# Performance work log

Measured on AMD Instinct MI355X. Metric: run time of the kernel, lower is better.

The kernel has to match this reference:

```python
import jax, jax.numpy as jnp
import numpy as np

N_IMG = 256; N_PAD = 512; N_DELAYS = 32; N_GRID = 512
PIX = 4e-5; L_IMG = N_IMG * PIX
R_BODY = 0.008; V0 = 1500.0; GRID_HALF = 0.02
N_TH = 240; N_INT = 250; W0 = 30.0
LAM_TV = 1e-3; LAM_L1 = 1e-3

def _fourier_coord(n, l):
    f = np.fft.fftshift(np.fft.fftfreq(n, d=l / n))
    kx, ky = np.meshgrid(f, f, indexing='ij')
    k = 2.0 * np.pi * np.sqrt(kx ** 2 + ky ** 2)
    theta = np.mod(np.arctan2(ky, kx), 2.0 * np.pi)
    return k.astype(np.float32), theta.astype(np.float32)

_K2D, _TH2D = _fourier_coord(N_PAD, 2.0 * L_IMG)
K2D = jnp.asarray(_K2D)[None, None]            # [1,1,P,P]
TH2D = jnp.asarray(_TH2D)                      # [P,P]
MASK0 = jnp.asarray(((_TH2D >= 0.0) & (_TH2D <= 2 * np.pi)).astype(np.float32))
_THPI = np.mod(_TH2D + np.pi, 2 * np.pi)
MASK1 = jnp.asarray(((_THPI >= 0.0) & (_THPI <= 2 * np.pi)).astype(np.float32))
K_LOSS = jnp.asarray(np.fft.ifftshift(_K2D))[None, None]
_SIG = 0.0015 / PIX / np.sqrt(2.0 * np.log(2.0))   # gaussian window sigma (pixels)
_AX = np.arange(N_IMG) - (N_IMG - 1) / 2.0
_G = np.exp(-_AX ** 2 / (2.0 * _SIG ** 2))
GWIN = jnp.asarray(np.outer(_G, _G).astype(np.float32))[None]   # [1,N,N]
THETAS_WF = jnp.linspace(0.0, 2.0 * np.pi, N_TH, dtype=jnp.float32)   # [T]
STEPS = jnp.linspace(0.0, 1.0, N_INT, dtype=jnp.float32)[None]        # [1,S]


def _interp1d(xg, yg, xn):
    # linear interp on uniform grid xg (1D) of values yg; xn arbitrary shape
    dxg = xg[1] - xg[0]
    t = (xn - xg[0]) / dxg
    f = jnp.clip(jnp.floor(t).astype(jnp.int32), 0, xg.shape[0] - 1)
    c = jnp.clip(jnp.ceil(t).astype(jnp.int32), 0, xg.shape[0] - 1)
    yf, yc = yg[f], yg[c]
    denom = jnp.where(c == f, 1.0, xg[c] - xg[f])
    lin = yf + (yc - yf) * (xn - xg[f]) / denom
    return jnp.where(c == f, yc, lin)


def _wavefront(xq, yq, SoS, x_vec, y_vec):
    # time-of-flight wavefront: trapezoid quadrature of (1 - v0/SoS) along rays
    r = jnp.sqrt(xq ** 2 + yq ** 2)
    phi = jnp.arctan2(xq, yq)
    th = THETAS_WF[:, None]                      # [T,1]
    s = jnp.sin(th - phi)
    cd = jnp.cos(th - phi)                       # cos(phi - th) == cos(th - phi)
    disc = jnp.maximum(R_BODY ** 2 - (r * s) ** 2, 0.0)
    l_in = jnp.sqrt(disc) + r * cd
    l_out = 2.0 * jnp.sqrt(disc) * (cd >= 0.0).astype(jnp.float32)
    l = jnp.where(r < R_BODY, l_in, l_out)       # [T,1]
    dx = x_vec[1] - x_vec[0]
    dy = y_vec[1] - y_vec[0]
    xi = jnp.round((xq - l * STEPS * jnp.sin(th) - x_vec[0]) / dx).astype(jnp.int32)
    yi = jnp.round((yq - l * STEPS * jnp.cos(th) - y_vec[0]) / dy).astype(jnp.int32)
    fint = 1.0 - V0 / SoS[(-yi) % N_GRID, xi % N_GRID]   # [T,S] gather
    xs = l * STEPS                               # [T,S]
    wf = jnp.sum(0.5 * (fint[:, 1:] + fint[:, :-1]) * (xs[:, 1:] - xs[:, :-1]), axis=1)
    return THETAS_WF, wf


def _tf_pact(delays, thetas, wfs):
    w = _interp1d(thetas, wfs, TH2D)
    w_pi = _interp1d(thetas, wfs, jnp.mod(TH2D + jnp.pi, 2.0 * jnp.pi))
    d = delays.reshape(1, -1, 1, 1)
    tf = (jnp.exp(-1j * K2D * (d - w)) * MASK0 + jnp.exp(1j * K2D * (d - w_pi)) * MASK1) * 0.5
    return jnp.fft.ifftshift(tf, axes=(-2, -1))  # [1,D,P,P] complex


def _siren(x, W1, b1, W2, b2, W3, b3, W4, b4):
    h = jnp.sin(W0 * (x @ W1 + b1))
    h = jnp.sin(W0 * (h @ W2 + b2))
    h = jnp.sin(W0 * (h @ W3 + b3))
    return h @ W4 + b4


def _forward(W1, b1, W2, b2, W3, b3, W4, b4, y_img, delays, xq, yq,
             mgrid_masked, mask, mask_idx, x_vec, y_vec):
    out = _siren(mgrid_masked, W1, b1, W2, b2, W3, b3, W4, b4)[:, 0]
    SoS = jnp.full((N_GRID * N_GRID,), 1499.363, jnp.float32)
    SoS = SoS.at[mask_idx].set(out * 170.0 + 1550.0).reshape(N_GRID, N_GRID)
    thetas, wfs = _wavefront(xq[0], yq[0], SoS, x_vec, y_vec)
    H = _tf_pact(delays, thetas, wfs)
    yw = y_img * GWIN                                  # [1,D,N,N]
    pad = N_IMG // 2
    yp = jnp.pad(yw, ((0, 0), (0, 0), (pad, pad), (pad, pad)))
    Y = jnp.fft.fft2(jnp.fft.ifftshift(yp, axes=(-2, -1)))
    Ht = jnp.conj(H)
    HtH = jnp.abs(H) ** 2
    rhs = jnp.sum(Y * Ht, axis=-3, keepdims=True)
    lhs = jnp.sum(HtH, axis=-3, keepdims=True)
    X = rhs / lhs
    x_rec = jnp.fft.fftshift(jnp.fft.ifft2(X), axes=(-2, -1)).real
    data = jnp.mean((jnp.abs(Y) * K_LOSS - jnp.abs(H * X) * K_LOSS) ** 2, axis=(-3, -2, -1))
    tv = LAM_TV * (jnp.sum(jnp.abs((SoS[1:, :] - SoS[:-1, :]) * mask[1:, :]))
                   + jnp.sum(jnp.abs((SoS[:, 1:] - SoS[:, :-1]) * mask[:, 1:])))
    l1 = LAM_L1 * jnp.mean(jnp.abs(SoS - 1550.0) * mask)
    loss = data + tv + l1
    return x_rec, SoS, loss


def setup_inputs() -> dict:
    key = jax.random.key(0)
    ks = jax.random.split(key, 12)
    xg = np.linspace(-GRID_HALF, GRID_HALF, N_GRID).astype(np.float32)
    XX, YY = np.meshgrid(xg, xg, indexing='ij')
    mask_np = (XX ** 2 + YY ** 2 <= R_BODY ** 2).astype(np.float32)
    mask_idx = np.nonzero(mask_np.reshape(-1))[0].astype(np.int32)
    lin = np.linspace(-1.0, 1.0, N_GRID).astype(np.float32)
    GX, GY = np.meshgrid(lin, lin, indexing='ij')
    mgrid = np.stack([GX, GY], axis=-1).reshape(-1, 2)
    H = 128
    c = np.sqrt(6.0 / H) / W0
    def u(k, shape, b):
        return jax.random.uniform(k, shape, jnp.float32, -b, b)
    return {
        'W1': u(ks[0], (2, H), 0.5), 'b1': u(ks[1], (H,), 0.5),
        'W2': u(ks[2], (H, H), c), 'b2': u(ks[3], (H,), c),
        'W3': u(ks[4], (H, H), c), 'b3': u(ks[5], (H,), c),
        'W4': u(ks[6], (H, 1), c), 'b4': u(ks[7], (1,), c),
        'y_img': jax.random.normal(ks[8], (1, N_DELAYS, N_IMG, N_IMG), jnp.float32),
        'delays': jax.random.normal(ks[9], (N_DELAYS,), jnp.float32) * 5e-4,
        'xq': jnp.array([0.002], jnp.float32),
        'yq': jnp.array([0.001], jnp.float32),
        'mgrid_masked': jnp.asarray(mgrid[mask_idx]),
        'mask': jnp.asarray(mask_np),
        'mask_idx': jnp.asarray(mask_idx),
        'x_vec': jnp.asarray(xg),
        'y_vec': jnp.asarray(xg),
    }


def reference(W1, b1, W2, b2, W3, b3, W4, b4, y_img, delays, xq, yq,
              mgrid_masked, mask, mask_idx, x_vec, y_vec):
    return _forward(W1, b1, W2, b2, W3, b3, W4, b4, y_img, delays, xq, yq,
                    mgrid_masked, mask, mask_idx, x_vec, y_vec)
```

## Files before the change

kernel.cpp:

```cpp
#include <hip/hip_runtime.h>
#include <hip/hip_bf16.h>
#include <math.h>

#define NP 512
#define NIMG 256
#define NDEL 32
#define NTH 240
#define NINT 250
#define SOS_ELEMS (512*512)
#define MLP_P 32
#define PHY(i) ((i) + ((i) >> 3))
#define RSW 576
#define PI_F 3.14159265358979323846f

__device__ __forceinline__ int brev9(int i) { return (int)(__brev((unsigned)i) >> 23); }

__device__ __forceinline__ float block_reduce_any(float v) {
  #pragma unroll
  for (int o = 32; o > 0; o >>= 1) v += __shfl_down(v, o, 64);
  __shared__ float red[8];
  int lane = threadIdx.x & 63, wid = threadIdx.x >> 6;
  __syncthreads();
  if (lane == 0) red[wid] = v;
  __syncthreads();
  float r = 0.f;
  if (threadIdx.x == 0) {
    int nw = blockDim.x >> 6;
    for (int i = 0; i < nw; ++i) r += red[i];
  }
  return r;
}

__device__ __forceinline__ void r4_bfly(float2& x0, float2& x1, float2& x2, float2& x3,
                                        float c1, float s1n, float c2, float s2n, float sign) {
  float t1x = x1.x * c1 - x1.y * s1n, t1y = x1.x * s1n + x1.y * c1;
  float y0x = x0.x + t1x, y0y = x0.y + t1y;
  float y1x = x0.x - t1x, y1y = x0.y - t1y;
  float t3x = x3.x * c1 - x3.y * s1n, t3y = x3.x * s1n + x3.y * c1;
  float y2x = x2.x + t3x, y2y = x2.y + t3y;
  float y3x = x2.x - t3x, y3y = x2.y - t3y;
  float t2x = y2x * c2 - y2y * s2n, t2y = y2x * s2n + y2y * c2;
  float ux = y3x * c2 - y3y * s2n, uy = y3x * s2n + y3y * c2;
  float t4x = -sign * uy, t4y = sign * ux;
  x0 = make_float2(y0x + t2x, y0y + t2y);
  x2 = make_float2(y0x - t2x, y0y - t2y);
  x1 = make_float2(y1x + t4x, y1y + t4y);
  x3 = make_float2(y1x - t4x, y1y - t4y);
}

__device__ __forceinline__ void fft512_r4_fwd_rows(float2 (*s)[RSW], int tid) {
  #pragma unroll
  for (int pass = 0; pass < 4; ++pass) {
    const int sh = 2 * pass;
    const int h = 1 << sh;
    int p = tid & 127;
    int rbase = (tid >> 7) << 2;
    int j = p & (h - 1);
    int g = p >> sh;
    int base = (g << (sh + 2)) + j;
    int i0 = PHY(base), i1 = PHY(base + h), i2 = PHY(base + 2 * h), i3 = PHY(base + 3 * h);
    float ang1 = -PI_F * (float)j / (float)h;
    float s1n, c1; __sincosf(ang1, &s1n, &c1);
    float s2n, c2; __sincosf(0.5f * ang1, &s2n, &c2);
    #pragma unroll
    for (int rr = 0; rr < 4; ++rr) {
      int r = rbase + rr;
      float2 x0 = s[r][i0], x1 = s[r][i1], x2 = s[r][i2], x3 = s[r][i3];
      r4_bfly(x0, x1, x2, x3, c1, s1n, c2, s2n, -1.f);
      s[r][i0] = x0; s[r][i1] = x1; s[r][i2] = x2; s[r][i3] = x3;
    }
    __syncthreads();
  }
  {
    int p = tid;
    int i1 = PHY(p), i2 = PHY(p + 256);
    float ang = -PI_F * (float)p * (1.f / 256.f);
    float sn, cs; __sincosf(ang, &sn, &cs);
    #pragma unroll
    for (int r = 0; r < 8; ++r) {
      float2 a = s[r][i1], b = s[r][i2];
      float tr = b.x * cs - b.y * sn;
      float ti = b.x * sn + b.y * cs;
      s[r][i1] = make_float2(a.x + tr, a.y + ti);
      s[r][i2] = make_float2(a.x - tr, a.y - ti);
    }
    __syncthreads();
  }
}

__device__ __forceinline__ void fft512_r4_fwd_rows4(float2 (*s)[RSW], int tid) {
  #pragma unroll
  for (int pass = 0; pass < 4; ++pass) {
    const int sh = 2 * pass;
    const int h = 1 << sh;
    int p = tid & 127;
    int rbase = (tid >> 7) << 1;
    int j = p & (h - 1);
    int g = p >> sh;
    int base = (g << (sh + 2)) + j;
    int i0 = PHY(base), i1 = PHY(base + h), i2 = PHY(base + 2 * h), i3 = PHY(base + 3 * h);
    float ang1 = -PI_F * (float)j / (float)h;
    float s1n, c1; __sincosf(ang1, &s1n, &c1);
    float s2n, c2; __sincosf(0.5f * ang1, &s2n, &c2);
    #pragma unroll
    for (int rr = 0; rr < 2; ++rr) {
      int r = rbase + rr;
      float2 x0 = s[r][i0], x1 = s[r][i1], x2 = s[r][i2], x3 = s[r][i3];
      r4_bfly(x0, x1, x2, x3, c1, s1n, c2, s2n, -1.f);
      s[r][i0] = x0; s[r][i1] = x1; s[r][i2] = x2; s[r][i3] = x3;
    }
    __syncthreads();
  }
  {
    int p = tid;
    int i1 = PHY(p), i2 = PHY(p + 256);
    float ang = -PI_F * (float)p * (1.f / 256.f);
    float sn, cs; __sincosf(ang, &sn, &cs);
    #pragma unroll
    for (int r = 0; r < 4; ++r) {
      float2 a = s[r][i1], b = s[r][i2];
      float tr = b.x * cs - b.y * sn;
      float ti = b.x * sn + b.y * cs;
      s[r][i1] = make_float2(a.x + tr, a.y + ti);
      s[r][i2] = make_float2(a.x - tr, a.y - ti);
    }
    __syncthreads();
  }
}

__device__ __forceinline__ void fft512_r4_row(float2* s, int tid, float sign) {
  #pragma unroll
  for (int pass = 0; pass < 4; ++pass) {
    const int sh = 2 * pass;
    const int h = 1 << sh;
    if (tid < 128) {
      int j = tid & (h - 1);
      int g = tid >> sh;
      int base = (g << (sh + 2)) + j;
      int i0 = PHY(base), i1 = PHY(base + h), i2 = PHY(base + 2 * h), i3 = PHY(base + 3 * h);
      float ang1 = sign * PI_F * (float)j / (float)h;
      float s1n, c1; __sincosf(ang1, &s1n, &c1);
      float s2n, c2; __sincosf(0.5f * ang1, &s2n, &c2);
      float2 x0 = s[i0], x1 = s[i1], x2 = s[i2], x3 = s[i3];
      r4_bfly(x0, x1, x2, x3, c1, s1n, c2, s2n, sign);
      s[i0] = x0; s[i1] = x1; s[i2] = x2; s[i3] = x3;
    }
    __syncthreads();
  }
  {
    int i1 = PHY(tid), i2 = PHY(tid + 256);
    float ang = sign * PI_F * (float)tid * (1.f / 256.f);
    float sn, cs; __sincosf(ang, &sn, &cs);
    float2 a = s[i1], b = s[i2];
    float tr = b.x * cs - b.y * sn;
    float ti = b.x * sn + b.y * cs;
    s[i1] = make_float2(a.x + tr, a.y + ti);
    s[i2] = make_float2(a.x - tr, a.y - ti);
    __syncthreads();
  }
}

__global__ __launch_bounds__(128) void k_mlp(
    const float* __restrict__ W1, const float* __restrict__ b1,
    const float* __restrict__ W2, const float* __restrict__ b2,
    const float* __restrict__ W3, const float* __restrict__ b3,
    const float* __restrict__ W4v, const float* __restrict__ b4,
    const float* __restrict__ mgrid, const int* __restrict__ mask_idx,
    const float* __restrict__ mask, int M,
    float* __restrict__ sos, float* __restrict__ acc) {
  __shared__ float hbuf[MLP_P][132];
  __shared__ float wbuf[2][8][132];
  __shared__ float xy2[MLP_P][2];
  int tid = threadIdx.x;
  int base = blockIdx.x * MLP_P;
  if (tid < MLP_P * 2) {
    int p = tid >> 1, c = tid & 1;
    float v = 0.f;
    if (base + p < M) v = mgrid[(base + p) * 2 + c];
    xy2[p][c] = v;
  }
  if (blockIdx.x == 0 && tid < 4) acc[tid] = 0.f;
  for (int slab = blockIdx.x; slab < 1024; slab += gridDim.x) {
    #pragma unroll
    for (int e = 0; e < 2; ++e) {
      int t = slab * 256 + tid + e * 128;
      if (mask[t] == 0.f) sos[t] = 1499.363f;
    }
  }
  __syncthreads();
  for (int e = tid; e < MLP_P * 128; e += 128) {
    int p = e >> 7, j = e & 127;
    hbuf[p][j] = __sinf(30.f * (xy2[p][0] * W1[j] + xy2[p][1] * W1[128 + j] + b1[j]));
  }
  __syncthreads();

  int jg = tid & 15, pg = tid >> 4;
  int jA = jg * 4, jB = 64 + jg * 4;
  int p0 = pg * 4;
  int wr = tid >> 4, wc = (tid & 15) << 3;
  #pragma unroll
  for (int layer = 0; layer < 2; ++layer) {
    const float* Wg = layer ? W3 : W2;
    const float* bb = layer ? b3 : b2;
    float acr[4][8];
    #pragma unroll
    for (int i = 0; i < 4; ++i)
      #pragma unroll
      for (int j = 0; j < 8; ++j) acr[i][j] = 0.f;

    float4 pre1 = *(const float4*)&Wg[wr * 128 + wc];
    float4 pre2 = *(const float4*)&Wg[wr * 128 + wc + 4];
    for (int c = 0; c < 16; ++c) {
      *(float4*)&wbuf[c & 1][wr][wc] = pre1;
      *(float4*)&wbuf[c & 1][wr][wc + 4] = pre2;
      __syncthreads();
      if (c < 15) {
        pre1 = *(const float4*)&Wg[((c + 1) * 8 + wr) * 128 + wc];
        pre2 = *(const float4*)&Wg[((c + 1) * 8 + wr) * 128 + wc + 4];
      }
      int k0 = c * 8;
      float hreg[4][8];
      #pragma unroll
      for (int i = 0; i < 4; ++i) {
        float4 ha = *(const float4*)&hbuf[p0 + i][k0];
        float4 hb = *(const float4*)&hbuf[p0 + i][k0 + 4];
        hreg[i][0] = ha.x; hreg[i][1] = ha.y; hreg[i][2] = ha.z; hreg[i][3] = ha.w;
        hreg[i][4] = hb.x; hreg[i][5] = hb.y; hreg[i][6] = hb.z; hreg[i][7] = hb.w;
      }
      #pragma unroll
      for (int kk = 0; kk < 8; ++kk) {
        float4 wa = *(const float4*)&wbuf[c & 1][kk][jA];
        float4 wb = *(const float4*)&wbuf[c & 1][kk][jB];
        float w8[8] = {wa.x, wa.y, wa.z, wa.w, wb.x, wb.y, wb.z, wb.w};
        #pragma unroll
        for (int i = 0; i < 4; ++i) {
          float hv = hreg[i][kk];
          #pragma unroll
          for (int j = 0; j < 8; ++j) acr[i][j] += hv * w8[j];
        }
      }
    }
    float breg[8];
    #pragma unroll
    for (int j = 0; j < 4; ++j) { breg[j] = bb[jA + j]; breg[4 + j] = bb[jB + j]; }
    __syncthreads();
    #pragma unroll
    for (int i = 0; i < 4; ++i) {
      float o[8];
      #pragma unroll
      for (int j = 0; j < 8; ++j) o[j] = __sinf(30.f * (acr[i][j] + breg[j]));
      *(float4*)&hbuf[p0 + i][jA] = make_float4(o[0], o[1], o[2], o[3]);
      *(float4*)&hbuf[p0 + i][jB] = make_float4(o[4], o[5], o[6], o[7]);
    }
    __syncthreads();
  }
  {
    int p = tid >> 2, q = tid & 3;
    float s = 0.f;
    #pragma unroll
    for (int k = 0; k < 32; k += 4) {
      float4 h4 = *(const float4*)&hbuf[p][q * 32 + k];
      float4 w4 = *(const float4*)&W4v[q * 32 + k];
      s += h4.x * w4.x + h4.y * w4.y + h4.z * w4.z + h4.w * w4.w;
    }
    s += __shfl_down(s, 1, 64);
    s += __shfl_down(s, 2, 64);
    if (q == 0 && base + p < M)
      sos[mask_idx[base + p]] = (s + b4[0]) * 170.f + 1550.f;
  }
}

__global__ __launch_bounds__(256) void k_mid(
    const float* __restrict__ y_img, float2* __restrict__ bufA,
    const float* __restrict__ sos, const float* __restrict__ xq_p,
    const float* __restrict__ yq_p, const float* __restrict__ x_vec,
    const float* __restrict__ y_vec, float* __restrict__ wfs,
    const float* __restrict__ mask, float* __restrict__ acc) {
  __shared__ float2 s[4][RSW];
  int bid = blockIdx.x;
  int tid = threadIdx.x;
  if (bid < 1024) {
    int rt = bid & 31;
    int d = bid >> 5;
    const float INV2S2 = (float)(0.6931471805599453 / 1406.25);
    for (int e = tid; e < 2048; e += 256) {
      int i = e >> 8, c = e & 255;
      int r = rt * 8 + i;
      float axr = (float)r - 127.5f;
      float axc = (float)c - 127.5f;
      float g = __expf(-(axr * axr + axc * axc) * INV2S2);
      float val = y_img[((size_t)d << 16) + (r << 8) + c] * g;
      int p = i >> 1, comp = i & 1;
      ((float*)&s[p][PHY(brev9((c + 384) & 511))])[comp] = val;
      ((float*)&s[p][PHY(brev9(c + 128))])[comp] = 0.f;
    }
    __syncthreads();
    fft512_r4_fwd_rows4(s, tid);
    float2* outp = bufA + ((size_t)d << 17) + rt * 8;
    for (int e = tid; e < 2056; e += 256) {
      int i = e & 7, v = e >> 3;
      int p = i >> 1, comp = i & 1;
      float2 Zv = s[p][PHY(v)];
      float2 Zm = s[p][PHY((512 - v) & 511)];
      float2 Yv;
      if (comp == 0) Yv = make_float2(0.5f * (Zv.x + Zm.x), 0.5f * (Zv.y - Zm.y));
      else           Yv = make_float2(0.5f * (Zv.y + Zm.y), 0.5f * (Zm.x - Zv.x));
      outp[(size_t)v * 256 + i] = Yv;
    }
  } else if (bid < 1024 + NTH) {
    int i = bid - 1024;
    int j = tid;
    float xq = xq_p[0], yq = yq_p[0];
    float r = sqrtf(xq * xq + yq * yq);
    float phi = atan2f(xq, yq);
    float th = (float)((double)i * (2.0 * M_PI / 239.0));
    float sn = sinf(th - phi), cd = cosf(th - phi);
    const float R2 = 0.008f * 0.008f;
    float disc = fmaxf(R2 - (r * sn) * (r * sn), 0.f);
    float sq = sqrtf(disc);
    float l_in = sq + r * cd;
    float l_out = 2.f * sq * (cd >= 0.f ? 1.f : 0.f);
    float l = (r < 0.008f) ? l_in : l_out;
    float x0 = x_vec[0], dx = x_vec[1] - x_vec[0];
    float y0 = y_vec[0], dy = y_vec[1] - y_vec[0];
    float sinth = sinf(th), costh = cosf(th);
    float contrib = 0.f;
    if (j < NINT) {
      float sj = (float)j * (1.f / 249.f);
      int xi = (int)rintf((xq - l * sj * sinth - x0) / dx);
      int yi = (int)rintf((yq - l * sj * costh - y0) / dy);
      float sv = sos[(((-yi) & 511) << 9) + (xi & 511)];
      float f = 1.f - 1500.f / sv;
      float wgt = (j == 0 || j == NINT - 1) ? 0.5f : 1.f;
      contrib = wgt * f;
    }
    float tot = block_reduce_any(contrib);
    if (tid == 0) wfs[i] = tot * l * (1.f / 249.f);
  } else {
    int t = (bid - 1024 - NTH) * 256 + tid;
    float sv = sos[t];
    float m = mask[t];
    int i = t >> 9, j = t & 511;
    float tv = 0.f;
    if (i > 0) tv += fabsf((sv - sos[t - 512]) * m);
    if (j > 0) tv += fabsf((sv - sos[t - 1]) * m);
    float l1 = fabsf(sv - 1550.f) * m;
    float tvb = block_reduce_any(tv);
    float l1b = block_reduce_any(l1);
    if (tid == 0) {
      atomicAdd(&acc[1], tvb);
      atomicAdd(&acc[2], l1b);
    }
  }
}

__device__ __forceinline__ float interp_wf(const float* wfs, float xn) {
  const float dxg = (float)(2.0 * M_PI / 239.0);
  float t = xn / dxg;
  int f = (int)floorf(t); f = min(max(f, 0), 239);
  int c = (int)ceilf(t);  c = min(max(c, 0), 239);
  float yf = wfs[f], yc = wfs[c];
  if (c == f) return yc;
  float xgf = (float)f * dxg;
  return yf + (yc - yf) * (xn - xgf) / ((float)(c - f) * dxg);
}

__global__ __launch_bounds__(256) void k_colfft_deconv(
    const float2* __restrict__ bufA, const float* __restrict__ delays,
    const float* __restrict__ wfs_g, float2* __restrict__ Xo,
    float* __restrict__ acc) {
  __shared__ float2 s[8][RSW];
  __shared__ float wfs[NTH];
  __shared__ float dly[NDEL];
  int v = blockIdx.x;
  int tid = threadIdx.x;
  if (tid < NTH) wfs[tid] = wfs_g[tid];
  if (tid < NDEL) dly[tid] = delays[tid];
  __syncthreads();

  const float inv_nd = 1.f / 0.02048f;
  const float TWO_PI = 6.28318530717958647692f;
  float fy = (float)(v < 256 ? v : v - 512) * inv_nd;
  float kkA[2];
  float2 zw[2], zwpi[2];
  int up[2];
  #pragma unroll
  for (int uu = 0; uu < 2; ++uu) {
    int u = tid + 256 * uu;
    up[uu] = PHY(u);
    float fx = (float)(u < 256 ? u : u - 512) * inv_nd;
    float kk = TWO_PI * sqrtf(fx * fx + fy * fy);
    kkA[uu] = kk;
    float th = atan2f(fy, fx);
    if (th < 0.f) th += TWO_PI;
    float w = interp_wf(wfs, th);
    float thpi = th + PI_F;
    if (thpi >= TWO_PI) thpi -= TWO_PI;
    float wpi = interp_wf(wfs, thpi);
    float snw, csw; __sincosf(kk * w, &snw, &csw);
    zw[uu] = make_float2(csw, snw);
    float snp, csp; __sincosf(kk * wpi, &snp, &csp);
    zwpi[uu] = make_float2(csp, snp);
  }

  float rhsr[2] = {0.f, 0.f}, rhsi[2] = {0.f, 0.f}, lhs[2] = {0.f, 0.f};
  float sY2[2] = {0.f, 0.f}, sYH[2] = {0.f, 0.f};

  for (int c4 = 0; c4 < 4; ++c4) {
    __syncthreads();
    for (int e = tid; e < 2048; e += 256) {
      int ch = e >> 8, c = e & 255;
      float2 val = bufA[((size_t)(c4 * 8 + ch) << 17) + (size_t)v * 256 + c];
      s[ch][PHY(brev9((c + 384) & 511))] = val;
      s[ch][PHY(brev9(c + 128))] = make_float2(0.f, 0.f);
    }
    __syncthreads();
    fft512_r4_fwd_rows(s, tid);
    #pragma unroll
    for (int uu = 0; uu < 2; ++uu) {
      float kk = kkA[uu];
      float2 w0 = zw[uu], w1 = zwpi[uu];
      #pragma unroll
      for (int ch = 0; ch < 8; ++ch) {
        float dl = dly[c4 * 8 + ch];
        float sd, cd2;
        __sincosf(kk * dl, &sd, &cd2);
        float t0r = cd2 * w0.x + sd * w0.y;
        float t0i = cd2 * w0.y - sd * w0.x;
        float t1r = cd2 * w1.x + sd * w1.y;
        float t1i = sd * w1.x - cd2 * w1.y;
        float Hr = 0.5f * (t0r + t1r);
        float Hi = 0.5f * (t0i + t1i);
        float2 Yv = s[ch][up[uu]];
        rhsr[uu] += Yv.x * Hr + Yv.y * Hi;
        rhsi[uu] += Yv.y * Hr - Yv.x * Hi;
        float h2 = Hr * Hr + Hi * Hi;
        float y2 = Yv.x * Yv.x + Yv.y * Yv.y;
        lhs[uu] += h2;
        sY2[uu] += y2;
        sYH[uu] += sqrtf(y2 * h2);
      }
    }
  }
  float lw = (v == 0 || v == 256) ? 1.f : 2.f;
  float2 Xv[2];
  float lsum = 0.f;
  #pragma unroll
  for (int uu = 0; uu < 2; ++uu) {
    float Xr = rhsr[uu] / lhs[uu], Xi = rhsi[uu] / lhs[uu];
    Xv[uu] = make_float2(Xr, Xi);
    float aX = sqrtf(Xr * Xr + Xi * Xi);
    float kk2 = kkA[uu] * kkA[uu];
    lsum += kk2 * (sY2[uu] - 2.f * aX * sYH[uu] + aX * aX * lhs[uu]);
  }
  float bs = block_reduce_any(lsum * lw);
  if (threadIdx.x == 0) atomicAdd(&acc[0], bs);
  __syncthreads();
  float2* s0 = &s[0][0];
  s0[PHY(brev9(tid))] = Xv[0];
  s0[PHY(brev9(tid + 256))] = Xv[1];
  __syncthreads();
  fft512_r4_row(s0, tid, +1.f);
  const float sc = 1.f / 512.f;
  float2 o0 = s0[PHY(tid)], o1 = s0[PHY(tid + 256)];
  o0.x *= sc; o0.y *= sc; o1.x *= sc; o1.y *= sc;
  Xo[((size_t)tid << 9) + v] = o0;
  Xo[((size_t)(tid + 256) << 9) + v] = o1;
  if (v != 0 && v != 256) {
    int vm = 512 - v;
    Xo[((size_t)tid << 9) + vm] = make_float2(o0.x, -o0.y);
    Xo[((size_t)(tid + 256) << 9) + vm] = make_float2(o1.x, -o1.y);
  }
}

__global__ __launch_bounds__(256) void k_final_rows(const float2* __restrict__ buf,
                                                    float* __restrict__ xrec,
                                                    const float* __restrict__ acc,
                                                    float* __restrict__ lossout) {
  __shared__ float2 s[RSW];
  int arow = blockIdx.x;
  const float2* p = buf + ((size_t)arow << 9);
  int tid = threadIdx.x;
  if (arow == 0 && tid == 0)
    lossout[0] = acc[0] * (1.f / 8388608.f) + 1e-3f * acc[1] + 1e-3f * (acc[2] * (1.f / 262144.f));
  s[PHY(brev9(tid))] = p[tid];
  s[PHY(brev9(tid + 256))] = p[tid + 256];
  __syncthreads();
  fft512_r4_row(s, tid, +1.f);
  int orow = (arow + 256) & 511;
  const float sc = 1.f / 512.f;
  xrec[(orow << 9) + ((tid + 256) & 511)] = s[PHY(tid)].x * sc;
  xrec[(orow << 9) + (tid & 511)] = s[PHY(tid + 256)].x * sc;
}

extern "C" void kernel_launch(void* const* d_in, const int* in_sizes, int n_in,
                              void* d_out, int out_size, void* d_ws, size_t ws_size,
                              hipStream_t stream) {
  const float* W1 = (const float*)d_in[0];
  const float* b1 = (const float*)d_in[1];
  const float* W2 = (const float*)d_in[2];
  const float* b2 = (const float*)d_in[3];
  const float* W3 = (const float*)d_in[4];
  const float* b3 = (const float*)d_in[5];
  const float* W4 = (const float*)d_in[6];
  const float* b4 = (const float*)d_in[7];
  const float* y_img = (const float*)d_in[8];
  const float* delays = (const float*)d_in[9];
  const float* xq = (const float*)d_in[10];
  const float* yq = (const float*)d_in[11];
  const float* mgrid = (const float*)d_in[12];
  const float* mask = (const float*)d_in[13];
  const int* mask_idx = (const int*)d_in[14];
  const float* x_vec = (const float*)d_in[15];
  const float* y_vec = (const float*)d_in[16];
  const int M = in_sizes[14];
  const int nMlp = (M + MLP_P - 1) / MLP_P;

  float* out = (float*)d_out;
  float* xrec = out;
  float* sos = out + SOS_ELEMS;
  float* loss = out + 2 * SOS_ELEMS;

  char* wsb = (char*)d_ws;
  float* acc = (float*)wsb;
  float* wfs = (float*)(wsb + 1024);
  float2* bufA = (float2*)(wsb + 4096);
  float2* bufX = (float2*)(wsb + 4096 + (size_t)NDEL * 512 * 256 * sizeof(float2));

  k_mlp<<<nMlp, 128, 0, stream>>>(W1, b1, W2, b2, W3, b3, W4, b4,
                                  mgrid, mask_idx, mask, M, sos, acc);
  k_mid<<<1024 + NTH + 1024, 256, 0, stream>>>(y_img, bufA, sos, xq, yq,
                                               x_vec, y_vec, wfs, mask, acc);
  k_colfft_deconv<<<257, 256, 0, stream>>>(bufA, delays, wfs, bufX, acc);
  k_final_rows<<<512, 256, 0, stream>>>(bufX, xrec, acc, loss);
}
```

Before: 205.5 us.

## Process four delay groups concurrently per block in column FFT deconvolution

The column-FFT deconvolution kernel now launches 1024 threads per block, so four thread groups each load and FFT one group of 8 delay channels in parallel. Previously one 256-thread block looped over the four groups in sequence. The per-group partial sums go through shared memory and are combined, and the inverse FFT is done on a single row by the first 256 threads. The aim is more parallelism and better latency hiding for the 257-block grid, which underfills the GPU. The cost is 4x shared memory (about 147KB) per block, which may exceed the LDS limit or allow only one block per CU, plus idle threads during the reduction and inverse FFT.

```diff
diff --git a/kernel.cpp b/kernel.cpp
--- a/kernel.cpp
+++ b/kernel.cpp
@@ -18,7 +18,7 @@
 __device__ __forceinline__ float block_reduce_any(float v) {
   #pragma unroll
   for (int o = 32; o > 0; o >>= 1) v += __shfl_down(v, o, 64);
-  __shared__ float red[8];
+  __shared__ float red[16];
   int lane = threadIdx.x & 63, wid = threadIdx.x >> 6;
   __syncthreads();
   if (lane == 0) red[wid] = v;
@@ -48,13 +48,13 @@
   x3 = make_float2(y1x - t4x, y1y - t4y);
 }
 
-__device__ __forceinline__ void fft512_r4_fwd_rows(float2 (*s)[RSW], int tid) {
+__device__ __forceinline__ void fft512_r4_fwd_rows(float2 (*s)[RSW], int lt) {
   #pragma unroll
   for (int pass = 0; pass < 4; ++pass) {
     const int sh = 2 * pass;
     const int h = 1 << sh;
-    int p = tid & 127;
-    int rbase = (tid >> 7) << 2;
+    int p = lt & 127;
+    int rbase = (lt >> 7) << 2;
     int j = p & (h - 1);
     int g = p >> sh;
     int base = (g << (sh + 2)) + j;
@@ -72,7 +72,7 @@
     __syncthreads();
   }
   {
-    int p = tid;
+    int p = lt;
     int i1 = PHY(p), i2 = PHY(p + 256);
     float ang = -PI_F * (float)p * (1.f / 256.f);
     float sn, cs; __sincosf(ang, &sn, &cs);
@@ -365,17 +365,19 @@
   return yf + (yc - yf) * (xn - xgf) / ((float)(c - f) * dxg);
 }
 
-__global__ __launch_bounds__(256) void k_colfft_deconv(
+__global__ __launch_bounds__(1024) void k_colfft_deconv(
     const float2* __restrict__ bufA, const float* __restrict__ delays,
     const float* __restrict__ wfs_g, float2* __restrict__ Xo,
     float* __restrict__ acc) {
-  __shared__ float2 s[8][RSW];
+  __shared__ float2 s[4][8][RSW];
   __shared__ float wfs[NTH];
   __shared__ float dly[NDEL];
   int v = blockIdx.x;
   int tid = threadIdx.x;
+  int grp = tid >> 8;
+  int lt = tid & 255;
   if (tid < NTH) wfs[tid] = wfs_g[tid];
-  if (tid < NDEL) dly[tid] = delays[tid];
+  if (tid >= 512 && tid < 512 + NDEL) dly[tid - 512] = delays[tid - 512];
   __syncthreads();
 
   const float inv_nd = 1.f / 0.02048f;
@@ -386,7 +388,7 @@
   int up[2];
   #pragma unroll
   for (int uu = 0; uu < 2; ++uu) {
-    int u = tid + 256 * uu;
+    int u = lt + 256 * uu;
     up[uu] = PHY(u);
     float fx = (float)(u < 256 ? u : u - 512) * inv_nd;
     float kk = TWO_PI * sqrtf(fx * fx + fy * fy);
@@ -403,73 +405,124 @@
     zwpi[uu] = make_float2(csp, snp);
   }
 
+  const int c4 = grp;
+  for (int e = lt; e < 2048; e += 256) {
+    int ch = e >> 8, c = e & 255;
+    float2 val = bufA[((size_t)(c4 * 8 + ch) << 17) + (size_t)v * 256 + c];
+    s[grp][ch][PHY(brev9((c + 384) & 511))] = val;
+    s[grp][ch][PHY(brev9(c + 128))] = make_float2(0.f, 0.f);
+  }
+  __syncthreads();
+  fft512_r4_fwd_rows(s[grp], lt);
+
   float rhsr[2] = {0.f, 0.f}, rhsi[2] = {0.f, 0.f}, lhs[2] = {0.f, 0.f};
   float sY2[2] = {0.f, 0.f}, sYH[2] = {0.f, 0.f};
-
-  for (int c4 = 0; c4 < 4; ++c4) {
-    __syncthreads();
-    for (int e = tid; e < 2048; e += 256) {
-      int ch = e >> 8, c = e & 255;
-      float2 val = bufA[((size_t)(c4 * 8 + ch) << 17) + (size_t)v * 256 + c];
-      s[ch][PHY(brev9((c + 384) & 511))] = val;
-      s[ch][PHY(brev9(c + 128))] = make_float2(0.f, 0.f);
-    }
-    __syncthreads();
-    fft512_r4_fwd_rows(s, tid);
+  #pragma unroll
+  for (int uu = 0; uu < 2; ++uu) {
+    float kk = kkA[uu];
+    float2 w0 = zw[uu], w1 = zwpi[uu];
+    #pragma unroll
+    for (int ch = 0; ch < 8; ++ch) {
+      float dl = dly[c4 * 8 + ch];
+      float sd, cd2;
+      __sincosf(kk * dl, &sd, &cd2);
+      float t0r = cd2 * w0.x + sd * w0.y;
+      float t0i = cd2 * w0.y - sd * w0.x;
+      float t1r = cd2 * w1.x + sd * w1.y;
+      float t1i = sd * w1.x - cd2 * w1.y;
+      float Hr = 0.5f * (t0r + t1r);
+      float Hi = 0.5f * (t0i + t1i);
+      float2 Yv = s[grp][ch][up[uu]];
+      rhsr[uu] += Yv.x * Hr + Yv.y * Hi;
+      rhsi[uu] += Yv.y * Hr - Yv.x * Hi;
+      float h2 = Hr * Hr + Hi * Hi;
+      float y2 = Yv.x * Yv.x + Yv.y * Yv.y;
+      lhs[uu] += h2;
+      sY2[uu] += y2;
+      sYH[uu] += sqrtf(y2 * h2);
+    }
+  }
+  __syncthreads();
+
+  float* rb = (float*)&s[0][0][0];
+  #pragma unroll
+  for (int uu = 0; uu < 2; ++uu) {
+    int u = lt + 256 * uu;
+    rb[(grp * 5 + 0) * 512 + u] = rhsr[uu];
+    rb[(grp * 5 + 1) * 512 + u] = rhsi[uu];
+    rb[(grp * 5 + 2) * 512 + u] = lhs[uu];
+    rb[(grp * 5 + 3) * 512 + u] = sY2[uu];
+    rb[(grp * 5 + 4) * 512 + u] = sYH[uu];
+  }
+  __syncthreads();
+
+  float lw = (v == 0 || v == 256) ? 1.f : 2.f;
+  float lsum = 0.f;
+  float2 Xv[2];
+  if (tid < 256) {
     #pragma unroll
     for (int uu = 0; uu < 2; ++uu) {
-      float kk = kkA[uu];
-      float2 w0 = zw[uu], w1 = zwpi[uu];
+      int u = lt + 256 * uu;
+      float R = 0.f, I = 0.f, L = 0.f, Y2 = 0.f, YH = 0.f;
       #pragma unroll
-      for (int ch = 0; ch < 8; ++ch) {
-        float dl = dly[c4 * 8 + ch];
-        float sd, cd2;
-        __sincosf(kk * dl, &sd, &cd2);
-        float t0r = cd2 * w0.x + sd * w0.y;
-        float t0i = cd2 * w0.y - sd * w0.x;
-        float t1r = cd2 * w1.x + sd * w1.y;
-        float t1i = sd * w1.x - cd2 * w1.y;
-        float Hr = 0.5f * (t0r + t1r);
-        float Hi = 0.5f * (t0i + t1i);
-        float2 Yv = s[ch][up[uu]];
-        rhsr[uu] += Yv.x * Hr + Yv.y * Hi;
-        rhsi[uu] += Yv.y * Hr - Yv.x * Hi;
-        float h2 = Hr * Hr + Hi * Hi;
-        float y2 = Yv.x * Yv.x + Yv.y * Yv.y;
-        lhs[uu] += h2;
-        sY2[uu] += y2;
-        sYH[uu] += sqrtf(y2 * h2);
+      for (int g = 0; g < 4; ++g) {
+        R  += rb[(g * 5 + 0) * 512 + u];
+        I  += rb[(g * 5 + 1) * 512 + u];
+        L  += rb[(g * 5 + 2) * 512 + u];
+        Y2 += rb[(g * 5 + 3) * 512 + u];
+        YH += rb[(g * 5 + 4) * 512 + u];
       }
-    }
-  }
-  float lw = (v == 0 || v == 256) ? 1.f : 2.f;
-  float2 Xv[2];
-  float lsum = 0.f;
-  #pragma unroll
-  for (int uu = 0; uu < 2; ++uu) {
-    float Xr = rhsr[uu] / lhs[uu], Xi = rhsi[uu] / lhs[uu];
-    Xv[uu] = make_float2(Xr, Xi);
-    float aX = sqrtf(Xr * Xr + Xi * Xi);
-    float kk2 = kkA[uu] * kkA[uu];
-    lsum += kk2 * (sY2[uu] - 2.f * aX * sYH[uu] + aX * aX * lhs[uu]);
+      float Xr = R / L, Xi = I / L;
+      Xv[uu] = make_float2(Xr, Xi);
+      float aX = sqrtf(Xr * Xr + Xi * Xi);
+      float kk2 = kkA[uu] * kkA[uu];
+      lsum += kk2 * (Y2 - 2.f * aX * YH + aX * aX * L);
+    }
   }
   float bs = block_reduce_any(lsum * lw);
-  if (threadIdx.x == 0) atomicAdd(&acc[0], bs);
-  __syncthreads();
-  float2* s0 = &s[0][0];
-  s0[PHY(brev9(tid))] = Xv[0];
-  s0[PHY(brev9(tid + 256))] = Xv[1];
-  __syncthreads();
-  fft512_r4_row(s0, tid, +1.f);
-  const float sc = 1.f / 512.f;
-  float2 o0 = s0[PHY(tid)], o1 = s0[PHY(tid + 256)];
-  o0.x *= sc; o0.y *= sc; o1.x *= sc; o1.y *= sc;
-  Xo[((size_t)tid << 9) + v] = o0;
-  Xo[((size_t)(tid + 256) << 9) + v] = o1;
-  if (v != 0 && v != 256) {
-    int vm = 512 - v;
-    Xo[((size_t)tid << 9) + vm] = make_float2(o0.x, -o0.y);
-    Xo[((size_t)(tid + 256) << 9) + vm] = make_float2(o1.x, -o1.y);
+  if (tid == 0) atomicAdd(&acc[0], bs);
+
+  float2* s3 = &s[3][0][0];
+  if (tid < 256) {
+    s3[PHY(brev9(lt))] = Xv[0];
+    s3[PHY(brev9(lt + 256))] = Xv[1];
+  }
+  __syncthreads();
+  #pragma unroll
+  for (int pass = 0; pass < 4; ++pass) {
+    const int sh = 2 * pass;
+    const int h = 1 << sh;
+    if (tid < 128) {
+      int j = tid & (h - 1);
+      int g = tid >> sh;
+      int base = (g << (sh + 2)) + j;
+      int i0 = PHY(base), i1 = PHY(base + h), i2 = PHY(base + 2 * h), i3 = PHY(base + 3 * h);
+      float ang1 = PI_F * (float)j / (float)h;
+      float s1n, c1; __sincosf(ang1, &s1n, &c1);
+      float s2n, c2; __sincosf(0.5f * ang1, &s2n, &c2);
+      float2 x0 = s3[i0], x1 = s3[i1], x2 = s3[i2], x3 = s3[i3];
+      r4_bfly(x0, x1, x2, x3, c1, s1n, c2, s2n, +1.f);
+      s3[i0] = x0; s3[i1] = x1; s3[i2] = x2; s3[i3] = x3;
+    }
+    __syncthreads();
+  }
+  if (tid < 256) {
+    int i1 = PHY(lt), i2 = PHY(lt + 256);
+    float ang = PI_F * (float)lt * (1.f / 256.f);
+    float sn, cs; __sincosf(ang, &sn, &cs);
+    float2 a = s3[i1], b = s3[i2];
+    float tr = b.x * cs - b.y * sn;
+    float ti = b.x * sn + b.y * cs;
+    const float sc = 1.f / 512.f;
+    float2 o0 = make_float2((a.x + tr) * sc, (a.y + ti) * sc);
+    float2 o1 = make_float2((a.x - tr) * sc, (a.y - ti) * sc);
+    Xo[((size_t)lt << 9) + v] = o0;
+    Xo[((size_t)(lt + 256) << 9) + v] = o1;
+    if (v != 0 && v != 256) {
+      int vm = 512 - v;
+      Xo[((size_t)lt << 9) + vm] = make_float2(o0.x, -o0.y);
+      Xo[((size_t)(lt + 256) << 9) + vm] = make_float2(o1.x, -o1.y);
+    }
   }
 }
 
@@ -531,6 +584,6 @@
                                   mgrid, mask_idx, mask, M, sos, acc);
   k_mid<<<1024 + NTH + 1024, 256, 0, stream>>>(y_img, bufA, sos, xq, yq,
                                                x_vec, y_vec, wfs, mask, acc);
-  k_colfft_deconv<<<257, 256, 0, stream>>>(bufA, delays, wfs, bufX, acc);
+  k_colfft_deconv<<<257, 1024, 0, stream>>>(bufA, delays, wfs, bufX, acc);
   k_final_rows<<<512, 256, 0, stream>>>(bufX, xrec, acc, loss);
 }
```

New measurement: 206.2 us. No clear change (+0.3%).

## Split column-FFT deconvolution across delay groups with a separate finalize kernel

Applied to the files above, without the earlier changes.

The single column-FFT deconvolution kernel is split in two. The first kernel launches one block per (column, group of 8 delays), 1028 blocks instead of 257, and writes its partial sums in place into the input buffer: rhs real and imaginary parts, lhs, and the YH term. A second kernel adds the four partial sums, solves for X, finishes the loss term and runs the inverse column FFT. The aim is to replace the serial four-iteration channel loop in each block with more blocks, filling the GPU better. The cost is an extra launch and several MB of extra global traffic for the partial buffers.

```diff
diff --git a/kernel.cpp b/kernel.cpp
--- a/kernel.cpp
+++ b/kernel.cpp
@@ -18,7 +18,7 @@
 __device__ __forceinline__ float block_reduce_any(float v) {
   #pragma unroll
   for (int o = 32; o > 0; o >>= 1) v += __shfl_down(v, o, 64);
-  __shared__ float red[8];
+  __shared__ float red[16];
   int lane = threadIdx.x & 63, wid = threadIdx.x >> 6;
   __syncthreads();
   if (lane == 0) red[wid] = v;
@@ -48,13 +48,13 @@
   x3 = make_float2(y1x - t4x, y1y - t4y);
 }
 
-__device__ __forceinline__ void fft512_r4_fwd_rows(float2 (*s)[RSW], int tid) {
+__device__ __forceinline__ void fft512_r4_fwd_rows(float2 (*s)[RSW], int lt) {
   #pragma unroll
   for (int pass = 0; pass < 4; ++pass) {
     const int sh = 2 * pass;
     const int h = 1 << sh;
-    int p = tid & 127;
-    int rbase = (tid >> 7) << 2;
+    int p = lt & 127;
+    int rbase = (lt >> 7) << 2;
     int j = p & (h - 1);
     int g = p >> sh;
     int base = (g << (sh + 2)) + j;
@@ -72,7 +72,7 @@
     __syncthreads();
   }
   {
-    int p = tid;
+    int p = lt;
     int i1 = PHY(p), i2 = PHY(p + 256);
     float ang = -PI_F * (float)p * (1.f / 256.f);
     float sn, cs; __sincosf(ang, &sn, &cs);
@@ -365,17 +365,19 @@
   return yf + (yc - yf) * (xn - xgf) / ((float)(c - f) * dxg);
 }
 
-__global__ __launch_bounds__(256) void k_colfft_deconv(
-    const float2* __restrict__ bufA, const float* __restrict__ delays,
-    const float* __restrict__ wfs_g, float2* __restrict__ Xo,
+__global__ __launch_bounds__(256) void k_colfft_part(
+    float2* bufA,
+    const float* __restrict__ delays, const float* __restrict__ wfs_g,
     float* __restrict__ acc) {
   __shared__ float2 s[8][RSW];
   __shared__ float wfs[NTH];
-  __shared__ float dly[NDEL];
-  int v = blockIdx.x;
+  __shared__ float dly[8];
+  int b = blockIdx.x;
+  int v = b >> 2;
+  int h = b & 3;
   int tid = threadIdx.x;
   if (tid < NTH) wfs[tid] = wfs_g[tid];
-  if (tid < NDEL) dly[tid] = delays[tid];
+  if (tid < 8) dly[tid] = delays[h * 8 + tid];
   __syncthreads();
 
   const float inv_nd = 1.f / 0.02048f;
@@ -403,66 +405,100 @@
     zwpi[uu] = make_float2(csp, snp);
   }
 
+  for (int e = tid; e < 2048; e += 256) {
+    int ch = e >> 8, c = e & 255;
+    float2 val = bufA[((size_t)(h * 8 + ch) << 17) + (size_t)v * 256 + c];
+    s[ch][PHY(brev9((c + 384) & 511))] = val;
+    s[ch][PHY(brev9(c + 128))] = make_float2(0.f, 0.f);
+  }
+  __syncthreads();
+  fft512_r4_fwd_rows(s, tid);
+
   float rhsr[2] = {0.f, 0.f}, rhsi[2] = {0.f, 0.f}, lhs[2] = {0.f, 0.f};
   float sY2[2] = {0.f, 0.f}, sYH[2] = {0.f, 0.f};
-
-  for (int c4 = 0; c4 < 4; ++c4) {
-    __syncthreads();
-    for (int e = tid; e < 2048; e += 256) {
-      int ch = e >> 8, c = e & 255;
-      float2 val = bufA[((size_t)(c4 * 8 + ch) << 17) + (size_t)v * 256 + c];
-      s[ch][PHY(brev9((c + 384) & 511))] = val;
-      s[ch][PHY(brev9(c + 128))] = make_float2(0.f, 0.f);
-    }
-    __syncthreads();
-    fft512_r4_fwd_rows(s, tid);
-    #pragma unroll
-    for (int uu = 0; uu < 2; ++uu) {
-      float kk = kkA[uu];
-      float2 w0 = zw[uu], w1 = zwpi[uu];
-      #pragma unroll
-      for (int ch = 0; ch < 8; ++ch) {
-        float dl = dly[c4 * 8 + ch];
-        float sd, cd2;
-        __sincosf(kk * dl, &sd, &cd2);
-        float t0r = cd2 * w0.x + sd * w0.y;
-        float t0i = cd2 * w0.y - sd * w0.x;
-        float t1r = cd2 * w1.x + sd * w1.y;
-        float t1i = sd * w1.x - cd2 * w1.y;
-        float Hr = 0.5f * (t0r + t1r);
-        float Hi = 0.5f * (t0i + t1i);
-        float2 Yv = s[ch][up[uu]];
-        rhsr[uu] += Yv.x * Hr + Yv.y * Hi;
-        rhsi[uu] += Yv.y * Hr - Yv.x * Hi;
-        float h2 = Hr * Hr + Hi * Hi;
-        float y2 = Yv.x * Yv.x + Yv.y * Yv.y;
-        lhs[uu] += h2;
-        sY2[uu] += y2;
-        sYH[uu] += sqrtf(y2 * h2);
-      }
-    }
-  }
+  #pragma unroll
+  for (int uu = 0; uu < 2; ++uu) {
+    float kk = kkA[uu];
+    float2 w0 = zw[uu], w1 = zwpi[uu];
+    #pragma unroll
+    for (int ch = 0; ch < 8; ++ch) {
+      float dl = dly[ch];
+      float sd, cd2;
+      __sincosf(kk * dl, &sd, &cd2);
+      float t0r = cd2 * w0.x + sd * w0.y;
+      float t0i = cd2 * w0.y - sd * w0.x;
+      float t1r = cd2 * w1.x + sd * w1.y;
+      float t1i = sd * w1.x - cd2 * w1.y;
+      float Hr = 0.5f * (t0r + t1r);
+      float Hi = 0.5f * (t0i + t1i);
+      float2 Yv = s[ch][up[uu]];
+      rhsr[uu] += Yv.x * Hr + Yv.y * Hi;
+      rhsi[uu] += Yv.y * Hr - Yv.x * Hi;
+      float h2 = Hr * Hr + Hi * Hi;
+      float y2 = Yv.x * Yv.x + Yv.y * Yv.y;
+      lhs[uu] += h2;
+      sY2[uu] += y2;
+      sYH[uu] += sqrtf(y2 * h2);
+    }
+  }
+
   float lw = (v == 0 || v == 256) ? 1.f : 2.f;
+  float lsum = kkA[0] * kkA[0] * sY2[0] + kkA[1] * kkA[1] * sY2[1];
+  float bs = block_reduce_any(lsum * lw);
+  if (tid == 0) atomicAdd(&acc[0], bs);
+
+  float* fb = (float*)bufA;
+  #pragma unroll
+  for (int uu = 0; uu < 2; ++uu) {
+    int u = tid + 256 * uu;
+    size_t base = ((size_t)v << 9) + u;
+    fb[(((size_t)(h * 8 + 0)) << 18) + base] = rhsr[uu];
+    fb[(((size_t)(h * 8 + 1)) << 18) + base] = rhsi[uu];
+    fb[(((size_t)(h * 8 + 2)) << 18) + base] = lhs[uu];
+    fb[(((size_t)(h * 8 + 3)) << 18) + base] = sYH[uu];
+  }
+}
+
+__global__ __launch_bounds__(256) void k_colfft_fin(
+    const float* __restrict__ bufP, float2* __restrict__ Xo,
+    float* __restrict__ acc) {
+  __shared__ float2 s[RSW];
+  int v = blockIdx.x;
+  int tid = threadIdx.x;
+  const float inv_nd = 1.f / 0.02048f;
+  const float TWO_PI = 6.28318530717958647692f;
+  float fy = (float)(v < 256 ? v : v - 512) * inv_nd;
+  float lw = (v == 0 || v == 256) ? 1.f : 2.f;
+  float lsum = 0.f;
   float2 Xv[2];
-  float lsum = 0.f;
   #pragma unroll
   for (int uu = 0; uu < 2; ++uu) {
-    float Xr = rhsr[uu] / lhs[uu], Xi = rhsi[uu] / lhs[uu];
+    int u = tid + 256 * uu;
+    float fx = (float)(u < 256 ? u : u - 512) * inv_nd;
+    float kk2 = TWO_PI * TWO_PI * (fx * fx + fy * fy);
+    float R = 0.f, I = 0.f, L = 0.f, YH = 0.f;
+    size_t base = ((size_t)v << 9) + u;
+    #pragma unroll
+    for (int h = 0; h < 4; ++h) {
+      R  += bufP[(((size_t)(h * 8 + 0)) << 18) + base];
+      I  += bufP[(((size_t)(h * 8 + 1)) << 18) + base];
+      L  += bufP[(((size_t)(h * 8 + 2)) << 18) + base];
+      YH += bufP[(((size_t)(h * 8 + 3)) << 18) + base];
+    }
+    float Xr = R / L, Xi = I / L;
     Xv[uu] = make_float2(Xr, Xi);
     float aX = sqrtf(Xr * Xr + Xi * Xi);
-    float kk2 = kkA[uu] * kkA[uu];
-    lsum += kk2 * (sY2[uu] - 2.f * aX * sYH[uu] + aX * aX * lhs[uu]);
+    lsum += kk2 * (aX * aX * L - 2.f * aX * YH);
   }
   float bs = block_reduce_any(lsum * lw);
-  if (threadIdx.x == 0) atomicAdd(&acc[0], bs);
-  __syncthreads();
-  float2* s0 = &s[0][0];
-  s0[PHY(brev9(tid))] = Xv[0];
-  s0[PHY(brev9(tid + 256))] = Xv[1];
-  __syncthreads();
-  fft512_r4_row(s0, tid, +1.f);
+  if (tid == 0) atomicAdd(&acc[0], bs);
+
+  s[PHY(brev9(tid))] = Xv[0];
+  s[PHY(brev9(tid + 256))] = Xv[1];
+  __syncthreads();
+  fft512_r4_row(s, tid, +1.f);
   const float sc = 1.f / 512.f;
-  float2 o0 = s0[PHY(tid)], o1 = s0[PHY(tid + 256)];
+  float2 o0 = s[PHY(tid)], o1 = s[PHY(tid + 256)];
   o0.x *= sc; o0.y *= sc; o1.x *= sc; o1.y *= sc;
   Xo[((size_t)tid << 9) + v] = o0;
   Xo[((size_t)(tid + 256) << 9) + v] = o1;
@@ -531,6 +567,7 @@
                                   mgrid, mask_idx, mask, M, sos, acc);
   k_mid<<<1024 + NTH + 1024, 256, 0, stream>>>(y_img, bufA, sos, xq, yq,
                                                x_vec, y_vec, wfs, mask, acc);
-  k_colfft_deconv<<<257, 256, 0, stream>>>(bufA, delays, wfs, bufX, acc);
+  k_colfft_part<<<1028, 256, 0, stream>>>(bufA, delays, wfs, acc);
+  k_colfft_fin<<<257, 256, 0, stream>>>((const float*)bufA, bufX, acc);
   k_final_rows<<<512, 256, 0, stream>>>(bufX, xrec, acc, loss);
 }
```

Result: no change. 204.5 us (-0.5%).
